# Performance work log

Hardware: AMD Instinct MI355X
Metric: run time of the kernel (lower is better)

Reference implementation:

```python
import jax, jax.numpy as jnp
import numpy as np

B, L, LM_DIM, D, R, NUM_LAYERS, C = 32, 1024, 1024, 128, 3, 2, 8
N = B * L
E = 524288
LN_EPS = 1e-5


def setup_inputs() -> dict:
    key = jax.random.key(0)
    ks = jax.random.split(key, 16)
    inp = {
        'output': jax.random.normal(ks[0], (B, L, LM_DIM), dtype=jnp.float32),
        'edge_index': jax.random.randint(ks[1], (2, E), 0, N, dtype=jnp.int64),
        'edge_type': jax.random.randint(ks[2], (E,), 0, R, dtype=jnp.int64),
        'attention_mask': jax.random.randint(ks[3], (B, L), 0, 2, dtype=jnp.int64),
        'labels': jax.random.randint(ks[4], (B, L), 0, C, dtype=jnp.int64),
        # parameters
        'lm_W': jax.random.normal(ks[5], (D, LM_DIM), dtype=jnp.float32) * 0.02,
        'lm_b': jnp.zeros((D,), dtype=jnp.float32),
        'ln_g': jnp.ones((D,), dtype=jnp.float32),
        'ln_b': jnp.zeros((D,), dtype=jnp.float32),
        'W_rel': jax.random.normal(ks[6], (NUM_LAYERS, R, D, D), dtype=jnp.float32) * 0.05,
        'W_root': jax.random.normal(ks[7], (NUM_LAYERS, D, D), dtype=jnp.float32) * 0.05,
        'conv_b': jnp.zeros((NUM_LAYERS, D), dtype=jnp.float32),
        'cls_W': jax.random.normal(ks[8], (C, 2 * D), dtype=jnp.float32) * 0.05,
        'cls_b': jnp.zeros((C,), dtype=jnp.float32),
    }
    return inp


def _forward(output, edge_index, edge_type, attention_mask, labels,
             lm_W, lm_b, ln_g, ln_b, W_rel, W_root, conv_b, cls_W, cls_b):
    # LM head + ReLU (dropout is identity in eval) + LayerNorm
    lm = jax.nn.relu(jnp.einsum('bld,hd->blh', output, lm_W) + lm_b)
    mu = jnp.mean(lm, axis=-1, keepdims=True)
    var = jnp.mean(jnp.square(lm - mu), axis=-1, keepdims=True)
    lm = (lm - mu) * jax.lax.rsqrt(var + LN_EPS) * ln_g + ln_b  # [B,L,D]

    # RGCN over flattened nodes
    x = lm.reshape(N, D)
    src, dst = edge_index[0], edge_index[1]
    seg = dst * R + edge_type  # combined (node, relation) segment id
    ones = jnp.ones((E,), dtype=x.dtype)
    cnt = jax.ops.segment_sum(ones, seg, num_segments=N * R).reshape(N, R, 1)
    denom = jnp.maximum(cnt, 1.0)
    for layer in range(NUM_LAYERS):
        x_src = x[src]  # [E,D] gather
        sums = jax.ops.segment_sum(x_src, seg, num_segments=N * R).reshape(N, R, D)
        mean_r = sums / denom  # per-relation mean aggregation (PyG RGCNConv aggr='mean')
        out = jnp.einsum('nrd,rde->ne', mean_r, W_rel[layer])
        out = out + x @ W_root[layer] + conv_b[layer]
        x = jax.nn.relu(out)  # dropout identity

    g = x.reshape(B, L, D)
    feat = jnp.concatenate([lm, g], axis=-1)  # [B,L,2D]
    logits = jnp.einsum('blh,ch->blc', feat, cls_W) + cls_b  # [B,L,C]

    # masked cross-entropy (ignore where attention_mask != 1)
    valid = (attention_mask.reshape(-1) == 1)
    logp = jax.nn.log_softmax(logits.reshape(-1, C), axis=-1)
    nll = -jnp.take_along_axis(logp, labels.reshape(-1, 1), axis=1)[:, 0]
    n_valid = jnp.maximum(jnp.sum(valid.astype(logits.dtype)), 1.0)
    loss = jnp.sum(jnp.where(valid, nll, 0.0)) / n_valid
    return loss, logits


def reference(output, edge_index, edge_type, attention_mask, labels,
              lm_W, lm_b, ln_g, ln_b, W_rel, W_root, conv_b, cls_W, cls_b):
    return _forward(output, edge_index, edge_type, attention_mask, labels,
                    lm_W, lm_b, ln_g, ln_b, W_rel, W_root, conv_b, cls_W, cls_b)
```

## Files before the change

kernel.cpp:

```cpp
#include <hip/hip_runtime.h>

#define Bb 32
#define Ll 1024
#define LMD 1024
#define Dd 128
#define Rr 3
#define NLAYER 2
#define Cc 8
#define Nn (Bb*Ll)
#define Ee 524288
#define NSEG (Nn*Rr)
#define LN_EPS 1e-5f

typedef __attribute__((ext_vector_type(8))) short bf16x8;
typedef __attribute__((ext_vector_type(4))) float f32x4;

__device__ inline short f2bf(float f) {
    unsigned u = __builtin_bit_cast(unsigned, f);
    u += 0x7fff + ((u >> 16) & 1);
    return (short)(u >> 16);
}
__device__ inline float bf2f(unsigned short s) {
    unsigned u = ((unsigned)s) << 16;
    return __builtin_bit_cast(float, u);
}

__global__ __launch_bounds__(256) void pack_all_kernel(
    const float* __restrict__ lmW, const float* __restrict__ Wrel,
    const float* __restrict__ Wroot, short* __restrict__ Wp_all)
{
    int idx = blockIdx.x * 256 + threadIdx.x;
    float v;
    if (idx < 131072) {
        int kk = idx & 31, n = (idx >> 5) & 127, ks = idx >> 12;
        v = lmW[n * 1024 + ks * 32 + kk];
    } else {
        int j = idx - 131072;
        int layer = j >> 16;
        int kk = j & 31, n = (j >> 5) & 127, ks = (j >> 12) & 15;
        int k = ks * 32 + kk;
        v = (k < 384) ? Wrel[(size_t)layer * 49152 + (size_t)k * 128 + n]
                      : Wroot[(size_t)layer * 16384 + (size_t)(k - 384) * 128 + n];
    }
    Wp_all[idx] = f2bf(v);
}

__global__ __launch_bounds__(256) void lm_gemm_ln_kernel(
    const float* __restrict__ A,
    const short* __restrict__ Wp,
    const float* __restrict__ bias,
    const float* __restrict__ lng, const float* __restrict__ lnb,
    float* __restrict__ lm_f32, short* __restrict__ lm_bf16)
{
    const int wv   = threadIdx.x >> 6;
    const int lane = threadIdx.x & 63;
    const int m16  = lane & 15;
    const int quad = lane >> 4;
    const int row_frag = blockIdx.x * 64 + wv * 16 + m16;
    const float* arow = A + (size_t)row_frag * 1024 + quad * 8;

    f32x4 acc[8];
    #pragma unroll
    for (int i = 0; i < 8; ++i) acc[i] = (f32x4){0.f, 0.f, 0.f, 0.f};

    #pragma unroll 2
    for (int ks = 0; ks < 32; ++ks) {
        const short* wpb = Wp + ks * 4096 + m16 * 32 + quad * 8;
        bf16x8 bfr[8];
        #pragma unroll
        for (int nt = 0; nt < 8; ++nt)
            bfr[nt] = *(const bf16x8*)(wpb + nt * 512);
        const float4* ap = (const float4*)(arow + ks * 32);
        float4 a0 = ap[0], a1 = ap[1];
        union { bf16x8 v; short s[8]; } af;
        af.s[0] = f2bf(a0.x); af.s[1] = f2bf(a0.y);
        af.s[2] = f2bf(a0.z); af.s[3] = f2bf(a0.w);
        af.s[4] = f2bf(a1.x); af.s[5] = f2bf(a1.y);
        af.s[6] = f2bf(a1.z); af.s[7] = f2bf(a1.w);
        #pragma unroll
        for (int nt = 0; nt < 8; ++nt)
            acc[nt] = __builtin_amdgcn_mfma_f32_16x16x32_bf16(af.v, bfr[nt], acc[nt], 0, 0, 0);
    }

    float v[8][4];
    #pragma unroll
    for (int nt = 0; nt < 8; ++nt) {
        float bs = bias[nt * 16 + m16];
        #pragma unroll
        for (int r = 0; r < 4; ++r) v[nt][r] = fmaxf(acc[nt][r] + bs, 0.f);
    }
    float gv[8], bv[8];
    #pragma unroll
    for (int nt = 0; nt < 8; ++nt) { gv[nt] = lng[nt * 16 + m16]; bv[nt] = lnb[nt * 16 + m16]; }

    const int row0 = blockIdx.x * 64 + wv * 16 + quad * 4;
    #pragma unroll
    for (int r = 0; r < 4; ++r) {
        float s = 0.f;
        #pragma unroll
        for (int nt = 0; nt < 8; ++nt) s += v[nt][r];
        s += __shfl_xor(s, 1, 64); s += __shfl_xor(s, 2, 64);
        s += __shfl_xor(s, 4, 64); s += __shfl_xor(s, 8, 64);
        float mu = s * (1.f / 128.f);
        float q = 0.f;
        #pragma unroll
        for (int nt = 0; nt < 8; ++nt) { float d = v[nt][r] - mu; q += d * d; }
        q += __shfl_xor(q, 1, 64); q += __shfl_xor(q, 2, 64);
        q += __shfl_xor(q, 4, 64); q += __shfl_xor(q, 8, 64);
        float rs = rsqrtf(q * (1.f / 128.f) + LN_EPS);
        size_t rowoff = (size_t)(row0 + r) * 128;
        #pragma unroll
        for (int nt = 0; nt < 8; ++nt) {
            float o = (v[nt][r] - mu) * rs * gv[nt] + bv[nt];
            lm_f32[rowoff + nt * 16 + m16] = o;
            lm_bf16[rowoff + nt * 16 + m16] = f2bf(o);
        }
    }
}

__global__ __launch_bounds__(256) void conv_gemm_kernel(
    const short* __restrict__ A1,
    const short* __restrict__ A2,
    const short* __restrict__ Wp,
    const float* __restrict__ bias,
    short* __restrict__ out_bf16)
{
    const int wv   = threadIdx.x >> 6;
    const int lane = threadIdx.x & 63;
    const int m16  = lane & 15;
    const int quad = lane >> 4;
    const int row_frag = blockIdx.x * 64 + wv * 16 + m16;
    const short* a1row = A1 + (size_t)row_frag * 384 + quad * 8;
    const short* a2row = A2 + (size_t)row_frag * 128 + quad * 8;

    f32x4 acc[8];
    #pragma unroll
    for (int i = 0; i < 8; ++i) acc[i] = (f32x4){0.f, 0.f, 0.f, 0.f};

    #pragma unroll 2
    for (int ks = 0; ks < 16; ++ks) {
        const short* wpb = Wp + ks * 4096 + m16 * 32 + quad * 8;
        bf16x8 bfr[8];
        #pragma unroll
        for (int nt = 0; nt < 8; ++nt)
            bfr[nt] = *(const bf16x8*)(wpb + nt * 512);
        const short* ar = (ks < 12) ? (a1row + ks * 32) : (a2row + (ks - 12) * 32);
        bf16x8 af = *(const bf16x8*)ar;
        #pragma unroll
        for (int nt = 0; nt < 8; ++nt)
            acc[nt] = __builtin_amdgcn_mfma_f32_16x16x32_bf16(af, bfr[nt], acc[nt], 0, 0, 0);
    }

    const int row0 = blockIdx.x * 64 + wv * 16 + quad * 4;
    #pragma unroll
    for (int nt = 0; nt < 8; ++nt) {
        float bs = bias[nt * 16 + m16];
        #pragma unroll
        for (int r = 0; r < 4; ++r) {
            float o = fmaxf(acc[nt][r] + bs, 0.f);
            out_bf16[(size_t)(row0 + r) * 128 + nt * 16 + m16] = f2bf(o);
        }
    }
}

__global__ __launch_bounds__(256) void hist_kernel(
    const int* __restrict__ dst, const int* __restrict__ et, int* __restrict__ counts)
{
    int e = blockIdx.x * 256 + threadIdx.x;
    atomicAdd(&counts[dst[e] * 3 + et[e]], 1);
}

__global__ __launch_bounds__(1024) void scan_kernel(
    const int* __restrict__ counts, int* __restrict__ row_ptr)
{
    __shared__ int sums[1024];
    const int t = threadIdx.x;
    const int CH = NSEG / 1024;
    int base = t * CH;
    int s = 0;
    for (int i = 0; i < CH; ++i) s += counts[base + i];
    sums[t] = s;
    __syncthreads();
    for (int off = 1; off < 1024; off <<= 1) {
        int v = sums[t];
        int add = (t >= off) ? sums[t - off] : 0;
        __syncthreads();
        sums[t] = v + add;
        __syncthreads();
    }
    int run = (t == 0) ? 0 : sums[t - 1];
    for (int i = 0; i < CH; ++i) { row_ptr[base + i] = run; run += counts[base + i]; }
    if (t == 1023) row_ptr[NSEG] = run;
}

__global__ __launch_bounds__(256) void scatter_kernel(
    const int* __restrict__ src, const int* __restrict__ dst, const int* __restrict__ et,
    const int* __restrict__ row_ptr, int* __restrict__ fill, int* __restrict__ edge_src)
{
    int e = blockIdx.x * 256 + threadIdx.x;
    int s = dst[e] * 3 + et[e];
    int pos = row_ptr[s] + atomicAdd(&fill[s], 1);
    edge_src[pos] = src[e];
}

__global__ __launch_bounds__(256) void aggregate_kernel(
    const short* __restrict__ x, const int* __restrict__ row_ptr,
    const int* __restrict__ edge_src, short* __restrict__ agg)
{
    int seg  = blockIdx.x * 4 + (threadIdx.x >> 6);
    int lane = threadIdx.x & 63;
    int b = row_ptr[seg], e = row_ptr[seg + 1];
    int n = seg / 3, r = seg - n * 3;
    float ax = 0.f, ay = 0.f;
    int i = b;
    for (; i + 2 <= e; i += 2) {
        int s0 = edge_src[i], s1 = edge_src[i + 1];
        unsigned u0 = *(const unsigned*)(x + (size_t)s0 * 128 + lane * 2);
        unsigned u1 = *(const unsigned*)(x + (size_t)s1 * 128 + lane * 2);
        ax += bf2f((unsigned short)(u0 & 0xffff)) + bf2f((unsigned short)(u1 & 0xffff));
        ay += bf2f((unsigned short)(u0 >> 16))    + bf2f((unsigned short)(u1 >> 16));
    }
    if (i < e) {
        int s0 = edge_src[i];
        unsigned u0 = *(const unsigned*)(x + (size_t)s0 * 128 + lane * 2);
        ax += bf2f((unsigned short)(u0 & 0xffff));
        ay += bf2f((unsigned short)(u0 >> 16));
    }
    int cnt = e - b;
    float inv = 1.f / (float)(cnt > 0 ? cnt : 1);
    unsigned short lo = (unsigned short)f2bf(ax * inv);
    unsigned short hi = (unsigned short)f2bf(ay * inv);
    *(unsigned*)(agg + (size_t)n * 384 + r * 128 + lane * 2) = (unsigned)lo | ((unsigned)hi << 16);
}

__global__ __launch_bounds__(256) void cls_loss_kernel(
    const float* __restrict__ lm, const short* __restrict__ g,
    const float* __restrict__ clsW, const float* __restrict__ clsb,
    const int* __restrict__ mask, const int* __restrict__ labels,
    float* __restrict__ logits, float* __restrict__ accb)
{
    __shared__ float W[2048];
    for (int i = threadIdx.x; i < 2048; i += 256) W[i] = clsW[i];
    __syncthreads();
    int n = blockIdx.x * 256 + threadIdx.x;
    float l[8];
    #pragma unroll
    for (int c = 0; c < 8; ++c) l[c] = clsb[c];
    const float* lmr = lm + (size_t)n * 128;
    const short* gr  = g  + (size_t)n * 128;
    #pragma unroll 4
    for (int h = 0; h < 128; h += 4) {
        float4 a = *(const float4*)(lmr + h);
        #pragma unroll
        for (int c = 0; c < 8; ++c) {
            const float* w = &W[c * 256 + h];
            l[c] = fmaf(a.x, w[0], l[c]); l[c] = fmaf(a.y, w[1], l[c]);
            l[c] = fmaf(a.z, w[2], l[c]); l[c] = fmaf(a.w, w[3], l[c]);
        }
    }
    #pragma unroll 2
    for (int h = 0; h < 128; h += 8) {
        uint4 raw = *(const uint4*)(gr + h);
        float a[8];
        a[0] = bf2f((unsigned short)(raw.x & 0xffff)); a[1] = bf2f((unsigned short)(raw.x >> 16));
        a[2] = bf2f((unsigned short)(raw.y & 0xffff)); a[3] = bf2f((unsigned short)(raw.y >> 16));
        a[4] = bf2f((unsigned short)(raw.z & 0xffff)); a[5] = bf2f((unsigned short)(raw.z >> 16));
        a[6] = bf2f((unsigned short)(raw.w & 0xffff)); a[7] = bf2f((unsigned short)(raw.w >> 16));
        #pragma unroll
        for (int c = 0; c < 8; ++c) {
            const float* w = &W[c * 256 + 128 + h];
            #pragma unroll
            for (int j = 0; j < 8; ++j) l[c] = fmaf(a[j], w[j], l[c]);
        }
    }
    #pragma unroll
    for (int c = 0; c < 8; ++c) logits[(size_t)n * 8 + c] = l[c];

    float m = l[0];
    #pragma unroll
    for (int c = 1; c < 8; ++c) m = fmaxf(m, l[c]);
    float ss = 0.f;
    #pragma unroll
    for (int c = 0; c < 8; ++c) ss += expf(l[c] - m);
    float lse = m + logf(ss);
    int y = labels[n];
    float ly = l[0];
    #pragma unroll
    for (int c = 1; c < 8; ++c) ly = (y == c) ? l[c] : ly;
    float nll = lse - ly;
    bool valid = (mask[n] == 1);
    float lv = valid ? nll : 0.f;
    float cv = valid ? 1.f : 0.f;
    #pragma unroll
    for (int off = 32; off > 0; off >>= 1) {
        lv += __shfl_down(lv, off, 64);
        cv += __shfl_down(cv, off, 64);
    }
    if ((threadIdx.x & 63) == 0) { atomicAdd(&accb[0], lv); atomicAdd(&accb[1], cv); }
}

__global__ void finalize_kernel(const float* __restrict__ accb, float* __restrict__ out)
{
    out[0] = accb[0] / fmaxf(accb[1], 1.f);
}

extern "C" void kernel_launch(void* const* d_in, const int* in_sizes, int n_in,
                              void* d_out, int out_size, void* d_ws, size_t ws_size,
                              hipStream_t stream)
{
    const float* output = (const float*)d_in[0];
    const int* edge_index = (const int*)d_in[1];
    const int* edge_type  = (const int*)d_in[2];
    const int* attn       = (const int*)d_in[3];
    const int* labels     = (const int*)d_in[4];
    const float* lmW   = (const float*)d_in[5];
    const float* lmb   = (const float*)d_in[6];
    const float* lng   = (const float*)d_in[7];
    const float* lnb   = (const float*)d_in[8];
    const float* Wrel  = (const float*)d_in[9];
    const float* Wroot = (const float*)d_in[10];
    const float* convb = (const float*)d_in[11];
    const float* clsW  = (const float*)d_in[12];
    const float* clsb  = (const float*)d_in[13];

    char* ws = (char*)d_ws;
    float* lm_f32 = (float*)ws;                          ws += (size_t)Nn * Dd * 4;
    short* lm_bf  = (short*)ws;                          ws += (size_t)Nn * Dd * 2;
    short* x1_bf  = (short*)ws;                          ws += (size_t)Nn * Dd * 2;
    short* x2_bf  = (short*)ws;                          ws += (size_t)Nn * Dd * 2;
    short* agg_bf = (short*)ws;                          ws += (size_t)Nn * 384 * 2;
    short* Wp_all = (short*)ws;                          ws += (size_t)262144 * 2;
    float* accb   = (float*)ws;                          ws += 64;
    int* counts   = (int*)ws;                            ws += (size_t)NSEG * 4;
    int* fill     = (int*)ws;                            ws += (size_t)NSEG * 4;
    int* row_ptr  = (int*)ws;                            ws += (size_t)(NSEG + 4) * 4;
    int* edge_src = (int*)ws;

    short* Wp_lm = Wp_all;
    short* Wp_c0 = Wp_all + 131072;
    short* Wp_c1 = Wp_all + 131072 + 65536;

    const int* e_src = edge_index;
    const int* e_dst = edge_index + Ee;

    hipMemsetAsync(accb, 0, 64 + 2 * (size_t)NSEG * 4, stream);

    pack_all_kernel<<<dim3(1024), dim3(256), 0, stream>>>(lmW, Wrel, Wroot, Wp_all);

    lm_gemm_ln_kernel<<<dim3(Nn / 64), dim3(256), 0, stream>>>(
        output, Wp_lm, lmb, lng, lnb, lm_f32, lm_bf);

    hist_kernel<<<dim3(Ee / 256), dim3(256), 0, stream>>>(e_dst, edge_type, counts);
    scan_kernel<<<dim3(1), dim3(1024), 0, stream>>>(counts, row_ptr);
    scatter_kernel<<<dim3(Ee / 256), dim3(256), 0, stream>>>(
        e_src, e_dst, edge_type, row_ptr, fill, edge_src);

    aggregate_kernel<<<dim3(NSEG / 4), dim3(256), 0, stream>>>(lm_bf, row_ptr, edge_src, agg_bf);
    conv_gemm_kernel<<<dim3(Nn / 64), dim3(256), 0, stream>>>(
        agg_bf, lm_bf, Wp_c0, convb, x1_bf);
    aggregate_kernel<<<dim3(NSEG / 4), dim3(256), 0, stream>>>(x1_bf, row_ptr, edge_src, agg_bf);
    conv_gemm_kernel<<<dim3(Nn / 64), dim3(256), 0, stream>>>(
        agg_bf, x1_bf, Wp_c1, convb + Dd, x2_bf);

    float* logits = (float*)d_out + 1;
    cls_loss_kernel<<<dim3(Nn / 256), dim3(256), 0, stream>>>(
        lm_f32, x2_bf, clsW, clsb, attn, labels, logits, accb);
    finalize_kernel<<<dim3(1), dim3(1), 0, stream>>>(accb, (float*)d_out);
}
```

Baseline: 487.8 us.

## Replace single-block prefix scan with three-phase multi-block wavefront scan

The single-workgroup scan over all 98304 segment counts becomes a three-kernel scan. Block-level shuffle scans write local exclusive sums and per-block totals, one small block scans the 384 totals, and a final pass adds the block offsets. Spreading the work across the whole GPU replaces the serial per-thread loops over 96 strided elements. The cost is two extra kernel launches and a scratch array of exclusive sums.

```diff
diff --git a/kernel.cpp b/kernel.cpp
--- a/kernel.cpp
+++ b/kernel.cpp
@@ -170,27 +170,52 @@
     atomicAdd(&counts[dst[e] * 3 + et[e]], 1);
 }
 
-__global__ __launch_bounds__(1024) void scan_kernel(
-    const int* __restrict__ counts, int* __restrict__ row_ptr)
-{
-    __shared__ int sums[1024];
-    const int t = threadIdx.x;
-    const int CH = NSEG / 1024;
-    int base = t * CH;
-    int s = 0;
-    for (int i = 0; i < CH; ++i) s += counts[base + i];
-    sums[t] = s;
+__global__ __launch_bounds__(256) void scan_blk_kernel(
+    const int* __restrict__ counts, int* __restrict__ excl, int* __restrict__ blksum)
+{
+    __shared__ int wsum[4];
+    int t = threadIdx.x, lane = t & 63, wv = t >> 6;
+    int g = blockIdx.x * 256 + t;
+    int v = counts[g];
+    int x = v;
+    #pragma unroll
+    for (int off = 1; off < 64; off <<= 1) {
+        int y = __shfl_up(x, off, 64);
+        if (lane >= off) x += y;
+    }
+    if (lane == 63) wsum[wv] = x;
     __syncthreads();
-    for (int off = 1; off < 1024; off <<= 1) {
-        int v = sums[t];
-        int add = (t >= off) ? sums[t - off] : 0;
-        __syncthreads();
-        sums[t] = v + add;
-        __syncthreads();
-    }
-    int run = (t == 0) ? 0 : sums[t - 1];
-    for (int i = 0; i < CH; ++i) { row_ptr[base + i] = run; run += counts[base + i]; }
-    if (t == 1023) row_ptr[NSEG] = run;
+    int woff = 0;
+    for (int i = 0; i < wv; ++i) woff += wsum[i];
+    excl[g] = woff + x - v;
+    if (t == 255) blksum[blockIdx.x] = woff + x;
+}
+
+__global__ __launch_bounds__(512) void scan_top_kernel(
+    const int* __restrict__ blksum, int* __restrict__ blkoff)
+{
+    __shared__ int wsum[8];
+    int t = threadIdx.x, lane = t & 63, wv = t >> 6;
+    int v = (t < 384) ? blksum[t] : 0;
+    int x = v;
+    #pragma unroll
+    for (int off = 1; off < 64; off <<= 1) {
+        int y = __shfl_up(x, off, 64);
+        if (lane >= off) x += y;
+    }
+    if (lane == 63) wsum[wv] = x;
+    __syncthreads();
+    int woff = 0;
+    for (int i = 0; i < wv; ++i) woff += wsum[i];
+    if (t < 384) blkoff[t] = woff + x - v;
+}
+
+__global__ __launch_bounds__(256) void scan_add_kernel(
+    const int* __restrict__ excl, const int* __restrict__ blkoff, int* __restrict__ row_ptr)
+{
+    int g = blockIdx.x * 256 + threadIdx.x;
+    row_ptr[g] = excl[g] + blkoff[blockIdx.x];
+    if (g == 0) row_ptr[NSEG] = Ee;
 }
 
 __global__ __launch_bounds__(256) void scatter_kernel(
@@ -334,6 +359,9 @@
     int* counts   = (int*)ws;                            ws += (size_t)NSEG * 4;
     int* fill     = (int*)ws;                            ws += (size_t)NSEG * 4;
     int* row_ptr  = (int*)ws;                            ws += (size_t)(NSEG + 4) * 4;
+    int* excl     = (int*)ws;                            ws += (size_t)NSEG * 4;
+    int* blksum   = (int*)ws;                            ws += 512 * 4;
+    int* blkoff   = (int*)ws;                            ws += 512 * 4;
     int* edge_src = (int*)ws;
 
     short* Wp_lm = Wp_all;
@@ -351,7 +379,9 @@
         output, Wp_lm, lmb, lng, lnb, lm_f32, lm_bf);
 
     hist_kernel<<<dim3(Ee / 256), dim3(256), 0, stream>>>(e_dst, edge_type, counts);
-    scan_kernel<<<dim3(1), dim3(1024), 0, stream>>>(counts, row_ptr);
+    scan_blk_kernel<<<dim3(NSEG / 256), dim3(256), 0, stream>>>(counts, excl, blksum);
+    scan_top_kernel<<<dim3(1), dim3(512), 0, stream>>>(blksum, blkoff);
+    scan_add_kernel<<<dim3(NSEG / 256), dim3(256), 0, stream>>>(excl, blkoff, row_ptr);
     scatter_kernel<<<dim3(Ee / 256), dim3(256), 0, stream>>>(
         e_src, e_dst, edge_type, row_ptr, fill, edge_src);
 
```

Result: faster. 455.6 us (-6.6%).
